# Optimization experiments

Hardware: AMD Instinct MI355X
Metric: run time of the kernel (lower is better)

## Reference

```python
import jax, jax.numpy as jnp
import numpy as np

NUM_NODES = 200000
NUM_EDGES = 4000000
NUM_GRAPHS = 512
D = 20
OUT = 5


def setup_inputs() -> dict:
    key = jax.random.key(0)
    k1, k2, k3, k4, k5, k6, k7 = jax.random.split(key, 7)
    x = jax.random.normal(k1, (NUM_NODES, D), dtype=jnp.float32)
    edge_index = jax.random.randint(k2, (2, NUM_EDGES), 0, NUM_NODES, dtype=jnp.int64)
    batch = jnp.sort(jax.random.randint(k3, (NUM_NODES,), 0, NUM_GRAPHS, dtype=jnp.int64))
    # GCNConv weight (glorot-ish) and bias; Linear(20 -> 5) weight/bias
    W1 = jax.random.normal(k4, (D, D), dtype=jnp.float32) / np.sqrt(D)
    b1 = jnp.zeros((D,), dtype=jnp.float32)
    W_out = jax.random.normal(k5, (D, OUT), dtype=jnp.float32) / np.sqrt(D)
    b_out = jax.random.normal(k6, (OUT,), dtype=jnp.float32) * 0.01
    return {"x": x, "edge_index": edge_index, "batch": batch,
            "W1": W1, "b1": b1, "W_out": W_out, "b_out": b_out}


def gcn_conv(x, edge_index, W, b, num_nodes):
    # PyG GCNConv: add self-loops, symmetric norm, linear transform, scatter-add, bias
    loop = jnp.arange(num_nodes, dtype=edge_index.dtype)
    src = jnp.concatenate([edge_index[0], loop])
    dst = jnp.concatenate([edge_index[1], loop])
    deg = jax.ops.segment_sum(jnp.ones_like(dst, dtype=x.dtype), dst, num_segments=num_nodes)
    dinv = jnp.where(deg > 0, jax.lax.rsqrt(deg), 0.0)
    norm = dinv[src] * dinv[dst]  # [E+N]
    h = x @ W                      # [N, D] transform first (cheaper than per-edge)
    msg = h[src] * norm[:, None]   # gather + scale  [E+N, D]
    out = jax.ops.segment_sum(msg, dst, num_segments=num_nodes)  # scatter-add
    return out + b


def reference(x, edge_index, batch, W1, b1, W_out, b_out):
    h = gcn_conv(x, edge_index, W1, b1, NUM_NODES)
    h = jax.nn.relu(h)
    # global mean pool per graph
    sums = jax.ops.segment_sum(h, batch, num_segments=NUM_GRAPHS)          # [G, D]
    cnts = jax.ops.segment_sum(jnp.ones((h.shape[0],), h.dtype), batch, num_segments=NUM_GRAPHS)
    pooled = sums / jnp.maximum(cnts, 1.0)[:, None]
    logits = pooled @ W_out + b_out                                        # [G, 5]
    return jax.nn.softmax(logits, axis=-1)
```

## Files before the change

### kernel.cpp

```cpp
#include <hip/hip_runtime.h>
#include <hip/hip_fp16.h>

#define N_NODES 200000
#define N_EDGES 4000000
#define N_GRAPHS 512
#define D 20
#define OUT 5

#define BSH 6
#define BN 64
#define NFB 3125
#define NFBP 3136
#define NBB 3129
#define NCB 49
#define NC 500
#define CHUNK 8000
#define CH2 7168
#define NCH2 13
#define MAX_EB 1792
#define GMAX 8

__launch_bounds__(1024)
__global__ void k_hist(const int* __restrict__ dst, int* __restrict__ hist_g,
                       float* __restrict__ gsum, int* __restrict__ bucket_tot) {
    __shared__ int h[NFBP];
    int t = threadIdx.x;
    if (blockIdx.x == 0) {
        for (int j = t; j < N_GRAPHS * D; j += 1024) gsum[j] = 0.f;
        for (int j = t; j < NFBP; j += 1024) bucket_tot[j] = 0;
    }
    for (int j = t; j < NFBP; j += 1024) h[j] = 0;
    __syncthreads();
    int base = blockIdx.x * CHUNK;
    for (int k = t; k < CHUNK; k += 1024) atomicAdd(&h[dst[base + k] >> BSH], 1);
    __syncthreads();
    for (int j = t; j < NFBP; j += 1024) hist_g[blockIdx.x * NFBP + j] = h[j];
}

__launch_bounds__(256)
__global__ void k_colsum(const int* __restrict__ hist_g, int* __restrict__ bucket_tot) {
    int col = blockIdx.x * 256 + threadIdx.x;
    if (col >= NFBP) return;
    int r0 = blockIdx.y * 50;
    int sum = 0;
    for (int r = r0; r < r0 + 50; r++) sum += hist_g[r * NFBP + col];
    if (sum) atomicAdd(&bucket_tot[col], sum);
}

__launch_bounds__(1024)
__global__ void k_scan_tot(const int* __restrict__ bucket_tot, int* __restrict__ bucket_base,
                           int* __restrict__ fcursor, int* __restrict__ ccursorA) {
    __shared__ int ps[1024];
    int t = threadIdx.x;
    int base = t * 4;
    int loc[4];
    int sum = 0;
    #pragma unroll
    for (int j = 0; j < 4; j++) {
        int idx = base + j;
        int x = (idx < NFBP) ? bucket_tot[idx] : 0;
        loc[j] = sum;
        sum += x;
    }
    ps[t] = sum;
    __syncthreads();
    for (int off = 1; off < 1024; off <<= 1) {
        int a = (t >= off) ? ps[t - off] : 0;
        __syncthreads();
        ps[t] += a;
        __syncthreads();
    }
    int carry = (t > 0) ? ps[t - 1] : 0;
    #pragma unroll
    for (int j = 0; j < 4; j++) {
        int idx = base + j;
        if (idx < NFBP) {
            int v = carry + loc[j];
            bucket_base[idx] = v;
            fcursor[idx] = v;
        }
    }
    __syncthreads();
    if (t < NCB) ccursorA[t] = bucket_base[t << 6];
}

__launch_bounds__(1024)
__global__ void k_partA(const int* __restrict__ src, const int* __restrict__ dst,
                        int* __restrict__ ccursorA, int* __restrict__ ebufA) {
    __shared__ int h[NCB];
    __shared__ int lcur[NCB];
    int t = threadIdx.x, c = blockIdx.x;
    if (t < NCB) h[t] = 0;
    __syncthreads();
    int base = c * CHUNK;
    for (int k = t; k < CHUNK; k += 1024) atomicAdd(&h[dst[base + k] >> 12], 1);
    __syncthreads();
    if (t < NCB) lcur[t] = atomicAdd(&ccursorA[t], h[t]);
    __syncthreads();
    for (int k = t; k < CHUNK; k += 1024) {
        int d = dst[base + k];
        int sv = src[base + k];
        int cb = d >> 12;
        int pos = atomicAdd(&lcur[cb], 1);
        ebufA[pos] = (sv << 12) | (d & 4095);
    }
}

__launch_bounds__(1024)
__global__ void k_partB(const int* __restrict__ ebufA, const int* __restrict__ bucket_base,
                        int* __restrict__ fcursor, int* __restrict__ ebuf) {
    int cb = blockIdx.x, j = blockIdx.y, t = threadIdx.x;
    int cbase = bucket_base[cb << 6];
    int cend_idx = (cb + 1) << 6; if (cend_idx > NFB) cend_idx = NFB;
    int cend = bucket_base[cend_idx];
    int lo = cbase + j * CH2;
    int hi = lo + CH2; if (hi > cend) hi = cend;
    if (lo >= hi) return;
    __shared__ int h[64];
    __shared__ int lcur[64];
    if (t < 64) h[t] = 0;
    __syncthreads();
    for (int k = lo + t; k < hi; k += 1024) atomicAdd(&h[(ebufA[k] >> 6) & 63], 1);
    __syncthreads();
    if (t < 64) lcur[t] = atomicAdd(&fcursor[(cb << 6) + t], h[t]);
    __syncthreads();
    for (int k = lo + t; k < hi; k += 1024) {
        int p = ebufA[k];
        int sb = (p >> 6) & 63;
        int pos = atomicAdd(&lcur[sb], 1);
        ebuf[pos] = ((p >> 12) << 6) | (p & 63);
    }
}

__launch_bounds__(256)
__global__ void k_count_xh(const int* __restrict__ ebuf, const int* __restrict__ bucket_base,
                           const float4* __restrict__ x4, int* __restrict__ offs_g,
                           uint2* __restrict__ xh2) {
    __shared__ int cnt[BN];
    __shared__ int s[BN];
    __shared__ float sdi[BN];
    int b = blockIdx.x, t = threadIdx.x;
    int eb = bucket_base[b], ee = bucket_base[b + 1];
    if (t < BN) cnt[t] = 0;
    __syncthreads();
    for (int k = eb + t; k < ee; k += 256) atomicAdd(&cnt[ebuf[k] & (BN - 1)], 1);
    __syncthreads();
    int nbn = N_NODES - (b << BSH); if (nbn > BN) nbn = BN;
    int v = (t < BN) ? cnt[t] : 0;
    if (t < BN) s[t] = v;
    __syncthreads();
    for (int off = 1; off < BN; off <<= 1) {
        int a = 0;
        if (t < BN && t >= off) a = s[t - off];
        __syncthreads();
        if (t < BN) s[t] += a;
        __syncthreads();
    }
    if (t < nbn) {
        int node = (b << BSH) + t;
        offs_g[node] = eb + s[t] - v;
        sdi[t] = rsqrtf((float)(v + 1));
    }
    __syncthreads();
    int nw = nbn * 5;
    for (int j = t; j < nw; j += 256) {
        int vl = j / 5, q = j - vl * 5;
        int node = (b << BSH) + vl;
        float4 xv = x4[node * 5 + q];
        float di = sdi[vl];
        __half2 h0 = __float22half2_rn(make_float2(xv.x * di, xv.y * di));
        __half2 h1 = __float22half2_rn(make_float2(xv.z * di, xv.w * di));
        uint2 u;
        u.x = *(unsigned int*)&h0;
        u.y = *(unsigned int*)&h1;
        xh2[node * 5 + q] = u;
    }
}

__launch_bounds__(256, 8)
__global__ void k_gather_fused(const int* __restrict__ ebuf, const int* __restrict__ bucket_base,
                               const int* __restrict__ offs_g, const uint2* __restrict__ xh2,
                               const int* __restrict__ batch, const float* __restrict__ W1,
                               const float* __restrict__ b1, float* __restrict__ gsum) {
    __shared__ int loff[BN + 1];
    __shared__ int cur[BN];
    __shared__ int lcsr[MAX_EB];
    __shared__ float w[D * D];
    __shared__ float wb[D];
    __shared__ float sagg[BN][21];
    __shared__ float lgsum[GMAX][D];
    int b = blockIdx.x, t = threadIdx.x;
    int eb = bucket_base[b], ee = bucket_base[b + 1];
    int n = ee - eb;
    int nbn = N_NODES - (b << BSH); if (nbn > BN) nbn = BN;

    for (int j = t; j < D * D; j += 256) w[j] = W1[j];
    if (t < D) wb[t] = b1[t];
    if (t < GMAX * D) ((float*)lgsum)[t] = 0.f;
    if (t < nbn) {
        int o = offs_g[(b << BSH) + t] - eb;
        loff[t] = o;
        cur[t] = o;
    }
    if (t == 0) loff[nbn] = n;
    __syncthreads();

    for (int k = t; k < n; k += 256) {
        int p = ebuf[eb + k];
        int pos = atomicAdd(&cur[p & (BN - 1)], 1);
        if (pos < MAX_EB) lcsr[pos] = p >> BSH;
    }
    __syncthreads();

    int nw = nbn * 5;
    for (int j = t; j < nw; j += 256) {
        int vl = j / 5, q = j - vl * 5;
        int node = (b << BSH) + vl;
        uint2 u = xh2[node * 5 + q];
        float2 a0 = __half22float2(*(__half2*)&u.x);
        float2 a1 = __half22float2(*(__half2*)&u.y);
        float accx = a0.x, accy = a0.y, accz = a1.x, accw = a1.y;
        float bccx = 0.f, bccy = 0.f, bccz = 0.f, bccw = 0.f;
        int lo = loff[vl], hi = loff[vl + 1];
        if (hi > MAX_EB) hi = MAX_EB;
        if (lo > MAX_EB) lo = MAX_EB;
        int k = lo;
        for (; k + 8 <= hi; k += 8) {
            int s0 = lcsr[k],     s1 = lcsr[k + 1], s2 = lcsr[k + 2], s3 = lcsr[k + 3];
            int s4 = lcsr[k + 4], s5 = lcsr[k + 5], s6 = lcsr[k + 6], s7 = lcsr[k + 7];
            uint2 m0 = xh2[s0 * 5 + q];
            uint2 m1 = xh2[s1 * 5 + q];
            uint2 m2 = xh2[s2 * 5 + q];
            uint2 m3 = xh2[s3 * 5 + q];
            uint2 m4 = xh2[s4 * 5 + q];
            uint2 m5 = xh2[s5 * 5 + q];
            uint2 m6 = xh2[s6 * 5 + q];
            uint2 m7 = xh2[s7 * 5 + q];
            float2 p0 = __half22float2(*(__half2*)&m0.x);
            float2 p1 = __half22float2(*(__half2*)&m0.y);
            float2 q0 = __half22float2(*(__half2*)&m1.x);
            float2 q1 = __half22float2(*(__half2*)&m1.y);
            float2 r0 = __half22float2(*(__half2*)&m2.x);
            float2 r1 = __half22float2(*(__half2*)&m2.y);
            float2 t0 = __half22float2(*(__half2*)&m3.x);
            float2 t1 = __half22float2(*(__half2*)&m3.y);
            accx += p0.x + q0.x; accy += p0.y + q0.y;
            accz += p1.x + q1.x; accw += p1.y + q1.y;
            bccx += r0.x + t0.x; bccy += r0.y + t0.y;
            bccz += r1.x + t1.x; bccw += r1.y + t1.y;
            float2 p2 = __half22float2(*(__half2*)&m4.x);
            float2 p3 = __half22float2(*(__half2*)&m4.y);
            float2 q2 = __half22float2(*(__half2*)&m5.x);
            float2 q3 = __half22float2(*(__half2*)&m5.y);
            float2 r2 = __half22float2(*(__half2*)&m6.x);
            float2 r3 = __half22float2(*(__half2*)&m6.y);
            float2 t2 = __half22float2(*(__half2*)&m7.x);
            float2 t3 = __half22float2(*(__half2*)&m7.y);
            accx += p2.x + q2.x; accy += p2.y + q2.y;
            accz += p3.x + q3.x; accw += p3.y + q3.y;
            bccx += r2.x + t2.x; bccy += r2.y + t2.y;
            bccz += r3.x + t3.x; bccw += r3.y + t3.y;
        }
        for (; k + 4 <= hi; k += 4) {
            int s0 = lcsr[k], s1 = lcsr[k + 1], s2 = lcsr[k + 2], s3 = lcsr[k + 3];
            uint2 m0 = xh2[s0 * 5 + q];
            uint2 m1 = xh2[s1 * 5 + q];
            uint2 m2 = xh2[s2 * 5 + q];
            uint2 m3 = xh2[s3 * 5 + q];
            float2 p0 = __half22float2(*(__half2*)&m0.x);
            float2 p1 = __half22float2(*(__half2*)&m0.y);
            float2 q0 = __half22float2(*(__half2*)&m1.x);
            float2 q1 = __half22float2(*(__half2*)&m1.y);
            float2 r0 = __half22float2(*(__half2*)&m2.x);
            float2 r1 = __half22float2(*(__half2*)&m2.y);
            float2 t0 = __half22float2(*(__half2*)&m3.x);
            float2 t1 = __half22float2(*(__half2*)&m3.y);
            accx += p0.x + q0.x; accy += p0.y + q0.y;
            accz += p1.x + q1.x; accw += p1.y + q1.y;
            bccx += r0.x + t0.x; bccy += r0.y + t0.y;
            bccz += r1.x + t1.x; bccw += r1.y + t1.y;
        }
        for (; k < hi; k++) {
            int sv = lcsr[k];
            uint2 m = xh2[sv * 5 + q];
            float2 m0 = __half22float2(*(__half2*)&m.x);
            float2 m1 = __half22float2(*(__half2*)&m.y);
            accx += m0.x; accy += m0.y; accz += m1.x; accw += m1.y;
        }
        sagg[vl][q * 4 + 0] = accx + bccx;
        sagg[vl][q * 4 + 1] = accy + bccy;
        sagg[vl][q * 4 + 2] = accz + bccz;
        sagg[vl][q * 4 + 3] = accw + bccw;
    }
    __syncthreads();

    int g0 = batch[b << BSH];
    int glast = batch[(b << BSH) + nbn - 1];
    int gcnt = glast - g0 + 1;

    if (t < nbn) {
        int node = (b << BSH) + t;
        float di = rsqrtf((float)(loff[t + 1] - loff[t] + 1));
        int gi = batch[node] - g0;
        float pre[D];
        #pragma unroll
        for (int d = 0; d < D; d++) pre[d] = sagg[t][d];
        int t20 = t % D;
        bool fits = (gcnt <= GMAX);
        for (int jj = 0; jj < D; jj++) {
            int o = t20 + jj; if (o >= D) o -= D;
            float h = 0.f;
            #pragma unroll
            for (int d = 0; d < D; d++) h = fmaf(pre[d], w[d * D + o], h);
            h = fmaf(h, di, wb[o]);
            h = fmaxf(h, 0.f);
            if (fits) atomicAdd(&lgsum[gi][o], h);
            else atomicAdd(&gsum[(g0 + gi) * D + o], h);
        }
    }
    __syncthreads();
    if (gcnt <= GMAX && t < gcnt * D) {
        atomicAdd(&gsum[(g0 + t / D) * D + (t % D)], lgsum[t / D][t % D]);
    }
}

__launch_bounds__(64)
__global__ void k_head(const float* __restrict__ gsum, const int* __restrict__ batch,
                       const float* __restrict__ W_out, const float* __restrict__ b_out,
                       float* __restrict__ out) {
    __shared__ float wo[D * OUT];
    __shared__ float bo[OUT];
    int t = threadIdx.x;
    for (int j = t; j < D * OUT; j += 64) wo[j] = W_out[j];
    if (t < OUT) bo[t] = b_out[t];
    __syncthreads();
    int g = blockIdx.x * 64 + t;
    if (g >= N_GRAPHS) return;
    auto lb = [&](int key) {
        int lo = 0, hi = N_NODES;
        while (lo < hi) { int mid = (lo + hi) >> 1; if (batch[mid] < key) lo = mid + 1; else hi = mid; }
        return lo;
    };
    int cnt = lb(g + 1) - lb(g);
    float inv = 1.0f / fmaxf((float)cnt, 1.0f);
    float logits[OUT];
    #pragma unroll
    for (int o = 0; o < OUT; o++) logits[o] = bo[o];
    #pragma unroll
    for (int d = 0; d < D; d++) {
        float p = gsum[g * D + d] * inv;
        #pragma unroll
        for (int o = 0; o < OUT; o++) logits[o] = fmaf(p, wo[d * OUT + o], logits[o]);
    }
    float m = logits[0];
    #pragma unroll
    for (int o = 1; o < OUT; o++) m = fmaxf(m, logits[o]);
    float ex[OUT], sum = 0.f;
    #pragma unroll
    for (int o = 0; o < OUT; o++) { ex[o] = __expf(logits[o] - m); sum += ex[o]; }
    float isum = 1.0f / sum;
    #pragma unroll
    for (int o = 0; o < OUT; o++) out[g * OUT + o] = ex[o] * isum;
}

extern "C" void kernel_launch(void* const* d_in, const int* in_sizes, int n_in,
                              void* d_out, int out_size, void* d_ws, size_t ws_size,
                              hipStream_t stream) {
    const float* x     = (const float*)d_in[0];
    const int*   edge  = (const int*)d_in[1];
    const int*   batch = (const int*)d_in[2];
    const float* W1    = (const float*)d_in[3];
    const float* b1    = (const float*)d_in[4];
    const float* W_out = (const float*)d_in[5];
    const float* b_out = (const float*)d_in[6];
    float* out = (float*)d_out;

    const int* src = edge;
    const int* dst = edge + N_EDGES;
    char* ws = (char*)d_ws;

    int*   hist_g      = (int*)(ws);
    int*   bucket_tot  = (int*)(ws + 6272000);
    int*   bucket_base = (int*)(ws + 6284544);
    int*   fcursor     = (int*)(ws + 6297088);
    int*   ccursorA    = (int*)(ws + 6309632);
    float* gsum        = (float*)(ws + 6309888);
    int*   offs_g      = (int*)(ws + 6350848);
    uint2* xh2         = (uint2*)(ws + 7150848);
    int*   ebufA       = (int*)(ws + 15150848);
    int*   ebuf        = (int*)(ws + 31150848);

    k_hist<<<NC, 1024, 0, stream>>>(dst, hist_g, gsum, bucket_tot);
    k_colsum<<<dim3(13, 10), 256, 0, stream>>>(hist_g, bucket_tot);
    k_scan_tot<<<1, 1024, 0, stream>>>(bucket_tot, bucket_base, fcursor, ccursorA);
    k_partA<<<NC, 1024, 0, stream>>>(src, dst, ccursorA, ebufA);
    k_partB<<<dim3(NCB, NCH2), 1024, 0, stream>>>(ebufA, bucket_base, fcursor, ebuf);
    k_count_xh<<<NFB, 256, 0, stream>>>(ebuf, bucket_base, (const float4*)x, offs_g, xh2);
    k_gather_fused<<<NFB, 256, 0, stream>>>(ebuf, bucket_base, offs_g, xh2, batch, W1, b1, gsum);
    k_head<<<(N_GRAPHS + 63) / 64, 64, 0, stream>>>(gsum, batch, W_out, b_out, out);
}
```

Measured before the change: 153.2 us.

## Fuse histogram with coarse partition and widen fp16 gather rows to 48 bytes

Merges the fine histogram and the coarse partition pass into one kernel. The coarse region bases become fixed-capacity slots set up by a new init kernel, so the partition no longer waits on the global scan and dst is read one time fewer. The fp16 node rows are also repacked from five 8-byte pieces into three 16-byte pieces, zero-padded to 24 halves, and the gather block shrinks to 192 threads. This means fewer, wider loads per edge, at the cost of padding bandwidth and an overflow cap (CAPA) that would silently drop edges for skewed inputs.

Result: slower. 162.3 us (+5.9%).

```diff
diff --git a/kernel.cpp b/kernel.cpp
--- a/kernel.cpp
+++ b/kernel.cpp
@@ -11,30 +11,55 @@
 #define BN 64
 #define NFB 3125
 #define NFBP 3136
-#define NBB 3129
 #define NCB 49
 #define NC 500
 #define CHUNK 8000
+#define CAPA 88064
 #define CH2 7168
 #define NCH2 13
 #define MAX_EB 1792
 #define GMAX 8
 
+__global__ void k_init(float* __restrict__ gsum, int* __restrict__ bucket_tot,
+                       int* __restrict__ ccursorA) {
+    int i = blockIdx.x * 256 + threadIdx.x;
+    if (i < N_GRAPHS * D) gsum[i] = 0.f;
+    else if (i < N_GRAPHS * D + NFBP) bucket_tot[i - N_GRAPHS * D] = 0;
+    else if (i < N_GRAPHS * D + NFBP + NCB) {
+        int cb = i - N_GRAPHS * D - NFBP;
+        ccursorA[cb] = cb * CAPA;
+    }
+}
+
 __launch_bounds__(1024)
-__global__ void k_hist(const int* __restrict__ dst, int* __restrict__ hist_g,
-                       float* __restrict__ gsum, int* __restrict__ bucket_tot) {
-    __shared__ int h[NFBP];
-    int t = threadIdx.x;
-    if (blockIdx.x == 0) {
-        for (int j = t; j < N_GRAPHS * D; j += 1024) gsum[j] = 0.f;
-        for (int j = t; j < NFBP; j += 1024) bucket_tot[j] = 0;
-    }
-    for (int j = t; j < NFBP; j += 1024) h[j] = 0;
-    __syncthreads();
-    int base = blockIdx.x * CHUNK;
-    for (int k = t; k < CHUNK; k += 1024) atomicAdd(&h[dst[base + k] >> BSH], 1);
-    __syncthreads();
-    for (int j = t; j < NFBP; j += 1024) hist_g[blockIdx.x * NFBP + j] = h[j];
+__global__ void k_histA(const int* __restrict__ src, const int* __restrict__ dst,
+                        int* __restrict__ hist_g, int* __restrict__ ccursorA,
+                        int* __restrict__ ebufA) {
+    __shared__ int hfine[NFBP];
+    __shared__ int hco[NCB];
+    __shared__ int lcur[NCB];
+    int t = threadIdx.x, c = blockIdx.x;
+    for (int j = t; j < NFBP; j += 1024) hfine[j] = 0;
+    __syncthreads();
+    int base = c * CHUNK;
+    for (int k = t; k < CHUNK; k += 1024) atomicAdd(&hfine[dst[base + k] >> BSH], 1);
+    __syncthreads();
+    if (t < NCB) {
+        int s = 0;
+        #pragma unroll 8
+        for (int i = 0; i < 64; i++) s += hfine[(t << 6) + i];
+        hco[t] = s;
+        lcur[t] = atomicAdd(&ccursorA[t], s);
+    }
+    for (int j = t; j < NFBP; j += 1024) hist_g[c * NFBP + j] = hfine[j];
+    __syncthreads();
+    for (int k = t; k < CHUNK; k += 1024) {
+        int d = dst[base + k];
+        int sv = src[base + k];
+        int cb = d >> 12;
+        int pos = atomicAdd(&lcur[cb], 1);
+        if (pos < (cb + 1) * CAPA) ebufA[pos] = (sv << 12) | (d & 4095);
+    }
 }
 
 __launch_bounds__(256)
@@ -49,7 +74,7 @@
 
 __launch_bounds__(1024)
 __global__ void k_scan_tot(const int* __restrict__ bucket_tot, int* __restrict__ bucket_base,
-                           int* __restrict__ fcursor, int* __restrict__ ccursorA) {
+                           int* __restrict__ fcursor) {
     __shared__ int ps[1024];
     int t = threadIdx.x;
     int base = t * 4;
@@ -80,41 +105,20 @@
             fcursor[idx] = v;
         }
     }
-    __syncthreads();
-    if (t < NCB) ccursorA[t] = bucket_base[t << 6];
 }
 
 __launch_bounds__(1024)
-__global__ void k_partA(const int* __restrict__ src, const int* __restrict__ dst,
-                        int* __restrict__ ccursorA, int* __restrict__ ebufA) {
-    __shared__ int h[NCB];
-    __shared__ int lcur[NCB];
-    int t = threadIdx.x, c = blockIdx.x;
-    if (t < NCB) h[t] = 0;
-    __syncthreads();
-    int base = c * CHUNK;
-    for (int k = t; k < CHUNK; k += 1024) atomicAdd(&h[dst[base + k] >> 12], 1);
-    __syncthreads();
-    if (t < NCB) lcur[t] = atomicAdd(&ccursorA[t], h[t]);
-    __syncthreads();
-    for (int k = t; k < CHUNK; k += 1024) {
-        int d = dst[base + k];
-        int sv = src[base + k];
-        int cb = d >> 12;
-        int pos = atomicAdd(&lcur[cb], 1);
-        ebufA[pos] = (sv << 12) | (d & 4095);
-    }
-}
-
-__launch_bounds__(1024)
-__global__ void k_partB(const int* __restrict__ ebufA, const int* __restrict__ bucket_base,
-                        int* __restrict__ fcursor, int* __restrict__ ebuf) {
+__global__ void k_partB(const int* __restrict__ ebufA, const int* __restrict__ ccursorA,
+                        const int* __restrict__ bucket_base, int* __restrict__ fcursor,
+                        int* __restrict__ ebuf) {
     int cb = blockIdx.x, j = blockIdx.y, t = threadIdx.x;
-    int cbase = bucket_base[cb << 6];
-    int cend_idx = (cb + 1) << 6; if (cend_idx > NFB) cend_idx = NFB;
-    int cend = bucket_base[cend_idx];
-    int lo = cbase + j * CH2;
-    int hi = lo + CH2; if (hi > cend) hi = cend;
+    int rbase = cb * CAPA;
+    int cnt = ccursorA[cb] - rbase;
+    if (cnt > CAPA) cnt = CAPA;
+    int lo = rbase + j * CH2;
+    int hi = lo + CH2;
+    int rend = rbase + cnt;
+    if (hi > rend) hi = rend;
     if (lo >= hi) return;
     __shared__ int h[64];
     __shared__ int lcur[64];
@@ -135,7 +139,7 @@
 __launch_bounds__(256)
 __global__ void k_count_xh(const int* __restrict__ ebuf, const int* __restrict__ bucket_base,
                            const float4* __restrict__ x4, int* __restrict__ offs_g,
-                           uint2* __restrict__ xh2) {
+                           uint4* __restrict__ xh48) {
     __shared__ int cnt[BN];
     __shared__ int s[BN];
     __shared__ float sdi[BN];
@@ -162,24 +166,37 @@
         sdi[t] = rsqrtf((float)(v + 1));
     }
     __syncthreads();
-    int nw = nbn * 5;
+    int nw = nbn * 3;
     for (int j = t; j < nw; j += 256) {
-        int vl = j / 5, q = j - vl * 5;
+        int vl = j / 3, q = j - vl * 3;
         int node = (b << BSH) + vl;
-        float4 xv = x4[node * 5 + q];
         float di = sdi[vl];
-        __half2 h0 = __float22half2_rn(make_float2(xv.x * di, xv.y * di));
-        __half2 h1 = __float22half2_rn(make_float2(xv.z * di, xv.w * di));
-        uint2 u;
-        u.x = *(unsigned int*)&h0;
-        u.y = *(unsigned int*)&h1;
-        xh2[node * 5 + q] = u;
-    }
-}
-
-__launch_bounds__(256, 8)
+        float4 lo4 = make_float4(0.f, 0.f, 0.f, 0.f), hi4 = lo4;
+        lo4 = x4[node * 5 + 2 * q];
+        if (q < 2) hi4 = x4[node * 5 + 2 * q + 1];
+        __half2 h0 = __float22half2_rn(make_float2(lo4.x * di, lo4.y * di));
+        __half2 h1 = __float22half2_rn(make_float2(lo4.z * di, lo4.w * di));
+        __half2 h2 = __float22half2_rn(make_float2(hi4.x * di, hi4.y * di));
+        __half2 h3 = __float22half2_rn(make_float2(hi4.z * di, hi4.w * di));
+        uint4 u;
+        u.x = *(unsigned int*)&h0; u.y = *(unsigned int*)&h1;
+        u.z = *(unsigned int*)&h2; u.w = *(unsigned int*)&h3;
+        xh48[node * 3 + q] = u;
+    }
+}
+
+__device__ __forceinline__ void acc4(float* a, unsigned lo, unsigned hi) {
+    float2 f0 = __half22float2(*(__half2*)&lo);
+    float2 f1 = __half22float2(*(__half2*)&hi);
+    a[0] += f0.x; a[1] += f0.y; a[2] += f1.x; a[3] += f1.y;
+}
+__device__ __forceinline__ void acc8(float* a, uint4 m) {
+    acc4(a, m.x, m.y); acc4(a + 4, m.z, m.w);
+}
+
+__launch_bounds__(192)
 __global__ void k_gather_fused(const int* __restrict__ ebuf, const int* __restrict__ bucket_base,
-                               const int* __restrict__ offs_g, const uint2* __restrict__ xh2,
+                               const int* __restrict__ offs_g, const uint4* __restrict__ xh48,
                                const int* __restrict__ batch, const float* __restrict__ W1,
                                const float* __restrict__ b1, float* __restrict__ gsum) {
     __shared__ int loff[BN + 1];
@@ -187,14 +204,14 @@
     __shared__ int lcsr[MAX_EB];
     __shared__ float w[D * D];
     __shared__ float wb[D];
-    __shared__ float sagg[BN][21];
+    __shared__ float sagg[BN][25];
     __shared__ float lgsum[GMAX][D];
     int b = blockIdx.x, t = threadIdx.x;
     int eb = bucket_base[b], ee = bucket_base[b + 1];
     int n = ee - eb;
     int nbn = N_NODES - (b << BSH); if (nbn > BN) nbn = BN;
 
-    for (int j = t; j < D * D; j += 256) w[j] = W1[j];
+    for (int j = t; j < D * D; j += 192) w[j] = W1[j];
     if (t < D) wb[t] = b1[t];
     if (t < GMAX * D) ((float*)lgsum)[t] = 0.f;
     if (t < nbn) {
@@ -205,22 +222,20 @@
     if (t == 0) loff[nbn] = n;
     __syncthreads();
 
-    for (int k = t; k < n; k += 256) {
+    for (int k = t; k < n; k += 192) {
         int p = ebuf[eb + k];
         int pos = atomicAdd(&cur[p & (BN - 1)], 1);
         if (pos < MAX_EB) lcsr[pos] = p >> BSH;
     }
     __syncthreads();
 
-    int nw = nbn * 5;
-    for (int j = t; j < nw; j += 256) {
-        int vl = j / 5, q = j - vl * 5;
+    int nw = nbn * 3;
+    for (int j = t; j < nw; j += 192) {
+        int vl = j / 3, q = j - vl * 3;
         int node = (b << BSH) + vl;
-        uint2 u = xh2[node * 5 + q];
-        float2 a0 = __half22float2(*(__half2*)&u.x);
-        float2 a1 = __half22float2(*(__half2*)&u.y);
-        float accx = a0.x, accy = a0.y, accz = a1.x, accw = a1.y;
-        float bccx = 0.f, bccy = 0.f, bccz = 0.f, bccw = 0.f;
+        float A[8] = {0.f, 0.f, 0.f, 0.f, 0.f, 0.f, 0.f, 0.f};
+        float B[8] = {0.f, 0.f, 0.f, 0.f, 0.f, 0.f, 0.f, 0.f};
+        acc8(A, xh48[node * 3 + q]);
         int lo = loff[vl], hi = loff[vl + 1];
         if (hi > MAX_EB) hi = MAX_EB;
         if (lo > MAX_EB) lo = MAX_EB;
@@ -228,69 +243,28 @@
         for (; k + 8 <= hi; k += 8) {
             int s0 = lcsr[k],     s1 = lcsr[k + 1], s2 = lcsr[k + 2], s3 = lcsr[k + 3];
             int s4 = lcsr[k + 4], s5 = lcsr[k + 5], s6 = lcsr[k + 6], s7 = lcsr[k + 7];
-            uint2 m0 = xh2[s0 * 5 + q];
-            uint2 m1 = xh2[s1 * 5 + q];
-            uint2 m2 = xh2[s2 * 5 + q];
-            uint2 m3 = xh2[s3 * 5 + q];
-            uint2 m4 = xh2[s4 * 5 + q];
-            uint2 m5 = xh2[s5 * 5 + q];
-            uint2 m6 = xh2[s6 * 5 + q];
-            uint2 m7 = xh2[s7 * 5 + q];
-            float2 p0 = __half22float2(*(__half2*)&m0.x);
-            float2 p1 = __half22float2(*(__half2*)&m0.y);
-            float2 q0 = __half22float2(*(__half2*)&m1.x);
-            float2 q1 = __half22float2(*(__half2*)&m1.y);
-            float2 r0 = __half22float2(*(__half2*)&m2.x);
-            float2 r1 = __half22float2(*(__half2*)&m2.y);
-            float2 t0 = __half22float2(*(__half2*)&m3.x);
-            float2 t1 = __half22float2(*(__half2*)&m3.y);
-            accx += p0.x + q0.x; accy += p0.y + q0.y;
-            accz += p1.x + q1.x; accw += p1.y + q1.y;
-            bccx += r0.x + t0.x; bccy += r0.y + t0.y;
-            bccz += r1.x + t1.x; bccw += r1.y + t1.y;
-            float2 p2 = __half22float2(*(__half2*)&m4.x);
-            float2 p3 = __half22float2(*(__half2*)&m4.y);
-            float2 q2 = __half22float2(*(__half2*)&m5.x);
-            float2 q3 = __half22float2(*(__half2*)&m5.y);
-            float2 r2 = __half22float2(*(__half2*)&m6.x);
-            float2 r3 = __half22float2(*(__half2*)&m6.y);
-            float2 t2 = __half22float2(*(__half2*)&m7.x);
-            float2 t3 = __half22float2(*(__half2*)&m7.y);
-            accx += p2.x + q2.x; accy += p2.y + q2.y;
-            accz += p3.x + q3.x; accw += p3.y + q3.y;
-            bccx += r2.x + t2.x; bccy += r2.y + t2.y;
-            bccz += r3.x + t3.x; bccw += r3.y + t3.y;
+            uint4 m0 = xh48[s0 * 3 + q];
+            uint4 m1 = xh48[s1 * 3 + q];
+            uint4 m2 = xh48[s2 * 3 + q];
+            uint4 m3 = xh48[s3 * 3 + q];
+            uint4 m4 = xh48[s4 * 3 + q];
+            uint4 m5 = xh48[s5 * 3 + q];
+            uint4 m6 = xh48[s6 * 3 + q];
+            uint4 m7 = xh48[s7 * 3 + q];
+            acc8(A, m0); acc8(B, m1); acc8(A, m2); acc8(B, m3);
+            acc8(A, m4); acc8(B, m5); acc8(A, m6); acc8(B, m7);
         }
         for (; k + 4 <= hi; k += 4) {
             int s0 = lcsr[k], s1 = lcsr[k + 1], s2 = lcsr[k + 2], s3 = lcsr[k + 3];
-            uint2 m0 = xh2[s0 * 5 + q];
-            uint2 m1 = xh2[s1 * 5 + q];
-            uint2 m2 = xh2[s2 * 5 + q];
-            uint2 m3 = xh2[s3 * 5 + q];
-            float2 p0 = __half22float2(*(__half2*)&m0.x);
-            float2 p1 = __half22float2(*(__half2*)&m0.y);
-            float2 q0 = __half22float2(*(__half2*)&m1.x);
-            float2 q1 = __half22float2(*(__half2*)&m1.y);
-            float2 r0 = __half22float2(*(__half2*)&m2.x);
-            float2 r1 = __half22float2(*(__half2*)&m2.y);
-            float2 t0 = __half22float2(*(__half2*)&m3.x);
-            float2 t1 = __half22float2(*(__half2*)&m3.y);
-            accx += p0.x + q0.x; accy += p0.y + q0.y;
-            accz += p1.x + q1.x; accw += p1.y + q1.y;
-            bccx += r0.x + t0.x; bccy += r0.y + t0.y;
-            bccz += r1.x + t1.x; bccw += r1.y + t1.y;
+            uint4 m0 = xh48[s0 * 3 + q];
+            uint4 m1 = xh48[s1 * 3 + q];
+            uint4 m2 = xh48[s2 * 3 + q];
+            uint4 m3 = xh48[s3 * 3 + q];
+            acc8(A, m0); acc8(B, m1); acc8(A, m2); acc8(B, m3);
         }
-        for (; k < hi; k++) {
-            int sv = lcsr[k];
-            uint2 m = xh2[sv * 5 + q];
-            float2 m0 = __half22float2(*(__half2*)&m.x);
-            float2 m1 = __half22float2(*(__half2*)&m.y);
-            accx += m0.x; accy += m0.y; accz += m1.x; accw += m1.y;
-        }
-        sagg[vl][q * 4 + 0] = accx + bccx;
-        sagg[vl][q * 4 + 1] = accy + bccy;
-        sagg[vl][q * 4 + 2] = accz + bccz;
-        sagg[vl][q * 4 + 3] = accw + bccw;
+        for (; k < hi; k++) acc8(A, xh48[lcsr[k] * 3 + q]);
+        #pragma unroll
+        for (int r = 0; r < 8; r++) sagg[vl][q * 8 + r] = A[r] + B[r];
     }
     __syncthreads();
 
@@ -379,23 +353,23 @@
     const int* dst = edge + N_EDGES;
     char* ws = (char*)d_ws;
 
-    int*   hist_g      = (int*)(ws);
-    int*   bucket_tot  = (int*)(ws + 6272000);
-    int*   bucket_base = (int*)(ws + 6284544);
-    int*   fcursor     = (int*)(ws + 6297088);
-    int*   ccursorA    = (int*)(ws + 6309632);
-    float* gsum        = (float*)(ws + 6309888);
-    int*   offs_g      = (int*)(ws + 6350848);
-    uint2* xh2         = (uint2*)(ws + 7150848);
-    int*   ebufA       = (int*)(ws + 15150848);
-    int*   ebuf        = (int*)(ws + 31150848);
-
-    k_hist<<<NC, 1024, 0, stream>>>(dst, hist_g, gsum, bucket_tot);
+    int*   bucket_tot  = (int*)(ws);
+    int*   bucket_base = (int*)(ws + 12544);
+    int*   fcursor     = (int*)(ws + 25088);
+    int*   ccursorA    = (int*)(ws + 37632);
+    float* gsum        = (float*)(ws + 37888);
+    int*   offs_g      = (int*)(ws + 78848);
+    uint4* xh48        = (uint4*)(ws + 878848);
+    int*   ebufA       = (int*)(ws + 10478848);
+    int*   ebuf        = (int*)(ws + 27739392);
+    int*   hist_g      = (int*)(ws + 43739392);
+
+    k_init<<<64, 256, 0, stream>>>(gsum, bucket_tot, ccursorA);
+    k_histA<<<NC, 1024, 0, stream>>>(src, dst, hist_g, ccursorA, ebufA);
     k_colsum<<<dim3(13, 10), 256, 0, stream>>>(hist_g, bucket_tot);
-    k_scan_tot<<<1, 1024, 0, stream>>>(bucket_tot, bucket_base, fcursor, ccursorA);
-    k_partA<<<NC, 1024, 0, stream>>>(src, dst, ccursorA, ebufA);
-    k_partB<<<dim3(NCB, NCH2), 1024, 0, stream>>>(ebufA, bucket_base, fcursor, ebuf);
-    k_count_xh<<<NFB, 256, 0, stream>>>(ebuf, bucket_base, (const float4*)x, offs_g, xh2);
-    k_gather_fused<<<NFB, 256, 0, stream>>>(ebuf, bucket_base, offs_g, xh2, batch, W1, b1, gsum);
+    k_scan_tot<<<1, 1024, 0, stream>>>(bucket_tot, bucket_base, fcursor);
+    k_partB<<<dim3(NCB, NCH2), 1024, 0, stream>>>(ebufA, ccursorA, bucket_base, fcursor, ebuf);
+    k_count_xh<<<NFB, 256, 0, stream>>>(ebuf, bucket_base, (const float4*)x, offs_g, xh48);
+    k_gather_fused<<<NFB, 192, 0, stream>>>(ebuf, bucket_base, offs_g, xh48, batch, W1, b1, gsum);
     k_head<<<(N_GRAPHS + 63) / 64, 64, 0, stream>>>(gsum, batch, W_out, b_out, out);
 }
```
